# Kernel tuning notes

Measured on AMD Instinct MI355X. Metric: run time of the kernel, lower is better.

## Reference

```python
import jax, jax.numpy as jnp
import numpy as np

B = 8192       # Monte Carlo paths
NSTEP = 30     # Euler time steps
D = 100        # z_dim / number of assets
H1 = 110
H2 = 110
T = NSTEP - 1  # number of subnets
DT = np.float32(1.0 / NSTEP)
R = np.float32(0.05)   # riskfree
EPS = np.float32(1e-3) # Keras BatchNormalization epsilon


def setup_inputs() -> dict:
    key = jax.random.key(0)
    ks = jax.random.split(key, 25)
    f = jnp.float32
    X = jax.random.normal(ks[0], (B, NSTEP, D), f)
    DWs = jax.random.normal(ks[1], (B, NSTEP, D), f) * jnp.sqrt(DT)
    sigmas = jax.random.uniform(ks[2], (D,), f, 0.1, 0.4)
    y_init = jax.random.uniform(ks[3], (1,), f, 0.0, 1.0)
    z_init = jax.random.uniform(ks[4], (1, D), f, -0.1, 0.1)
    W1 = jax.random.normal(ks[5], (T, D, H1), f) / np.sqrt(D).astype(np.float32)
    W2 = jax.random.normal(ks[6], (T, H1, H2), f) / np.sqrt(H1).astype(np.float32)
    W3 = jax.random.normal(ks[7], (T, H2, D), f) / np.sqrt(H2).astype(np.float32)
    dims = [D, H1, H2, D]
    bn = {}
    for j, dim in enumerate(dims):
        bn[f"g{j}"] = 1.0 + 0.1 * jax.random.normal(ks[8 + 4 * j], (T, dim), f)
        bn[f"b{j}"] = 0.05 * jax.random.normal(ks[9 + 4 * j], (T, dim), f)
        bn[f"m{j}"] = 0.1 * jax.random.normal(ks[10 + 4 * j], (T, dim), f)
        bn[f"v{j}"] = jax.random.uniform(ks[11 + 4 * j], (T, dim), f, 0.5, 1.5)
    return dict(X=X, DWs=DWs, sigmas=sigmas, y_init=y_init, z_init=z_init,
                W1=W1, W2=W2, W3=W3, **bn)


def _bn(x, g, b, m, v):
    # Keras BatchNormalization, inference mode
    return (x - m) * jax.lax.rsqrt(v + EPS) * g + b


def _subnet(x, p):
    (w1, w2, w3, g0, b0, m0, v0, g1, b1, m1, v1,
     g2, b2, m2, v2, g3, b3, m3, v3) = p
    x = _bn(x, g0, b0, m0, v0)
    x = jax.nn.relu(x @ w1)
    x = _bn(x, g1, b1, m1, v1)
    x = jax.nn.relu(x @ w2)
    x = _bn(x, g2, b2, m2, v2)
    x = x @ w3
    return _bn(x, g3, b3, m3, v3)


def reference(X, DWs, sigmas, y_init, z_init, W1, W2, W3,
              g0, b0, m0, v0, g1, b1, m1, v1,
              g2, b2, m2, v2, g3, b3, m3, v3):
    nb = X.shape[0]
    Y0 = jnp.ones((nb, 1), X.dtype) * y_init            # [B,1]
    Z0 = jnp.ones((nb, 1), X.dtype) * z_init            # [B,D]

    def step(carry, xs):
        Y, Z = carry
        Xi, Xn, DWi, p = xs
        Y = Y + R * Y * DT + jnp.sum(sigmas * Xi * Z * DWi, axis=1, keepdims=True)
        Z = _subnet(Xn, p)
        return (Y, Z), None

    params = (W1, W2, W3, g0, b0, m0, v0, g1, b1, m1, v1,
              g2, b2, m2, v2, g3, b3, m3, v3)  # each leading dim T
    xs = (jnp.moveaxis(X[:, :T], 1, 0),        # [T,B,D]
          jnp.moveaxis(X[:, 1:T + 1], 1, 0),   # [T,B,D]
          jnp.moveaxis(DWs[:, :T], 1, 0),      # [T,B,D]
          params)
    (Y, Z), _ = jax.lax.scan(step, (Y0, Z0), xs)
    # final step: X[:,-2,:] with DWs[:,-1,:]
    Y = Y + R * Y * DT + jnp.sum(sigmas * X[:, -2, :] * Z * DWs[:, -1, :],
                                 axis=1, keepdims=True)
    return Y
```

## Files before the change

kernel.cpp:

```cpp
#include <hip/hip_runtime.h>

typedef unsigned short ushort_t;
typedef __attribute__((ext_vector_type(8))) short s16x8;
typedef __attribute__((ext_vector_type(4))) float f32x4;

#define B_PATHS 8192
#define NSTEP   30
#define DD      100
#define HH      110
#define TT      29
#define ROWSTR  3000
#define LDK     136
#define WFRAGSZ 14336
#define DT_C    (1.0f/30.0f)
#define R_C     0.05f
#define EPS_C   1e-3f

__device__ __forceinline__ ushort_t f2bf(float f) {
  unsigned u = __float_as_uint(f);
  u = u + 0x7FFFu + ((u >> 16) & 1u);
  return (ushort_t)(u >> 16);
}
__device__ __forceinline__ float bf2f(ushort_t u) {
  return __uint_as_float(((unsigned)u) << 16);
}

__global__ void prep_kernel(const float* __restrict__ W1, const float* __restrict__ W2,
                            const float* __restrict__ W3,
                            const float* g0, const float* b0, const float* m0, const float* v0,
                            const float* g1, const float* b1, const float* m1, const float* v1,
                            const float* g2, const float* b2, const float* m2, const float* v2,
                            const float* g3, const float* b3, const float* m3, const float* v3,
                            ushort_t* __restrict__ wprep, float* __restrict__ bprep)
{
  const int mat = blockIdx.x, t = blockIdx.y, tid = threadIdx.x;
  __shared__ float wsh[110*110];
  __shared__ float sin_[112], hin_[112], sout_[112], hout_[112];

  int Kr, Nr; const float* W; const float *g, *bb, *mm, *vv;
  if (mat == 0)      { Kr = 100; Nr = 110; W = W1 + t*11000; g = g0+t*100; bb = b0+t*100; mm = m0+t*100; vv = v0+t*100; }
  else if (mat == 1) { Kr = 110; Nr = 110; W = W2 + t*12100; g = g1+t*110; bb = b1+t*110; mm = m1+t*110; vv = v1+t*110; }
  else               { Kr = 110; Nr = 100; W = W3 + t*11000; g = g2+t*110; bb = b2+t*110; mm = m2+t*110; vv = v2+t*110; }

  if (tid < Kr) {
    float s = g[tid] * rsqrtf(vv[tid] + EPS_C);
    sin_[tid] = s; hin_[tid] = bb[tid] - mm[tid]*s;
  }
  if (mat == 2 && tid < Nr) {
    float s = g3[t*100+tid] * rsqrtf(v3[t*100+tid] + EPS_C);
    sout_[tid] = s; hout_[tid] = b3[t*100+tid] - m3[t*100+tid]*s;
  }
  for (int i = tid; i < Kr*Nr; i += 256) wsh[i] = W[i];
  __syncthreads();

  if (tid < 128) {
    float c = 0.f;
    if (tid < Nr) {
      for (int k = 0; k < Kr; ++k) c += hin_[k] * wsh[k*Nr + tid];
      if (mat == 2) c = c * sout_[tid] + hout_[tid];
    }
    bprep[(t*3 + mat)*128 + tid] = c;
  }

  ushort_t* wo = wprep + (size_t)(t*3 + mat) * WFRAGSZ;
  for (int ch = tid; ch < 1792; ch += 256) {
    const int lane = ch & 63, ntkb = ch >> 6;
    const int nt = ntkb % 7, kb = ntkb / 7;
    const int n  = nt*16 + (lane & 15);
    const int k0 = kb*32 + (lane >> 4)*8;
    ushort_t tmp[8];
#pragma unroll
    for (int j = 0; j < 8; ++j) {
      const int k = k0 + j;
      float v = 0.f;
      if (n < Nr && k < Kr) {
        v = sin_[k] * wsh[k*Nr + n];
        if (mat == 2) v *= sout_[n];
      }
      tmp[j] = f2bf(v);
    }
    ushort4 lo; lo.x = tmp[0]; lo.y = tmp[1]; lo.z = tmp[2]; lo.w = tmp[3];
    ushort4 hi; hi.x = tmp[4]; hi.y = tmp[5]; hi.z = tmp[6]; hi.w = tmp[7];
    *(ushort4*)(wo + ch*8)     = lo;
    *(ushort4*)(wo + ch*8 + 4) = hi;
  }
}

__device__ __forceinline__ void mlp_stage(const ushort_t* actIn, const ushort_t* __restrict__ wfrag,
                                          const float* __restrict__ biasg, ushort_t* actOut,
                                          int lane, int lrow, int quad, bool relu)
{
  f32x4 acc[7];
  const f32x4 z4 = {0.f, 0.f, 0.f, 0.f};
#pragma unroll
  for (int nt = 0; nt < 7; ++nt) acc[nt] = z4;
  s16x8 a[4];
#pragma unroll
  for (int kb = 0; kb < 4; ++kb)
    a[kb] = *(const s16x8*)(actIn + lrow*LDK + kb*32 + quad*8);
#pragma unroll
  for (int kb = 0; kb < 4; ++kb) {
#pragma unroll
    for (int nt = 0; nt < 7; ++nt) {
      s16x8 b = *(const s16x8*)(wfrag + ((kb*7 + nt)*64 + lane)*8);
      acc[nt] = __builtin_amdgcn_mfma_f32_16x16x32_bf16(a[kb], b, acc[nt], 0, 0, 0);
    }
  }
  __asm__ volatile("" ::: "memory");
#pragma unroll
  for (int nt = 0; nt < 7; ++nt) {
    const int col = nt*16 + lrow;
    const float bv = biasg[col];
#pragma unroll
    for (int r = 0; r < 4; ++r) {
      float u = acc[nt][r] + bv;
      if (relu) u = u > 0.f ? u : 0.f;
      actOut[(quad*4 + r)*LDK + col] = f2bf(u);
    }
  }
#pragma unroll
  for (int r = 0; r < 4; ++r)
    actOut[(quad*4 + r)*LDK + 112 + lrow] = 0;
  __asm__ volatile("" ::: "memory");
}

__global__ __launch_bounds__(256, 4)
void subnet_kernel(const float* __restrict__ X, const float* __restrict__ DW,
                   const float* __restrict__ sigmas,
                   const ushort_t* __restrict__ wprep, const float* __restrict__ bprep,
                   float* __restrict__ sbuf)
{
  __shared__ __align__(16) ushort_t actA[4][16*LDK];
  __shared__ __align__(16) ushort_t actB[4][16*LDK];

  const int tid  = threadIdx.x;
  const int wv   = tid >> 6;
  const int t    = blockIdx.y;
  const int m0   = blockIdx.x * 64 + wv * 16;
  const int lane = tid & 63, lrow = lane & 15, quad = lane >> 4;
  const int row16 = lane >> 2, part = lane & 3;
  const int brow  = m0 + row16;

  ushort_t* A  = actA[wv];
  ushort_t* Bq = actB[wv];

  const float* drp = DW + (size_t)brow*ROWSTR + (t+1)*DD;
  float4 dwv[7];
#pragma unroll
  for (int g = 0; g < 7; ++g) {
    const int c = part + g*4;
    if (c < 25) dwv[g] = *(const float4*)(drp + c*4);
    else        { dwv[g].x = 0.f; dwv[g].y = 0.f; dwv[g].z = 0.f; dwv[g].w = 0.f; }
  }

  const float* xrp = X + (size_t)brow*ROWSTR + (t+1)*DD;
#pragma unroll
  for (int g = 0; g < 8; ++g) {
    const int c = part + g*4;
    ushort4 u; u.x = 0; u.y = 0; u.z = 0; u.w = 0;
    if (c < 25) {
      const float4 v = *(const float4*)(xrp + c*4);
      u.x = f2bf(v.x); u.y = f2bf(v.y); u.z = f2bf(v.z); u.w = f2bf(v.w);
    }
    *(ushort4*)(A + row16*LDK + c*4) = u;
  }
  __asm__ volatile("" ::: "memory");

  const ushort_t* wf = wprep + (size_t)(t*3) * WFRAGSZ;
  const float*    bg = bprep + (t*3) * 128;

  mlp_stage(A,  wf,             bg,       Bq, lane, lrow, quad, true);
  mlp_stage(Bq, wf + WFRAGSZ,   bg + 128, A,  lane, lrow, quad, true);
  mlp_stage(A,  wf + 2*WFRAGSZ, bg + 256, Bq, lane, lrow, quad, false);

  {
    const int xt = (t == TT - 1) ? (NSTEP - 2) : (t + 1);
    const float* xe = X + (size_t)brow*ROWSTR + xt*DD;
    float p = 0.f;
#pragma unroll
    for (int g = 0; g < 7; ++g) {
      const int c = part + g*4;
      if (c < 25) {
        const float4 xv = *(const float4*)(xe + c*4);
        const float4 sg = *(const float4*)(sigmas + c*4);
        const ushort4 zu = *(const ushort4*)(Bq + row16*LDK + c*4);
        p += sg.x*xv.x*dwv[g].x*bf2f(zu.x);
        p += sg.y*xv.y*dwv[g].y*bf2f(zu.y);
        p += sg.z*xv.z*dwv[g].z*bf2f(zu.z);
        p += sg.w*xv.w*dwv[g].w*bf2f(zu.w);
      }
    }
    p += __shfl_xor(p, 1, 64);
    p += __shfl_xor(p, 2, 64);
    if (part == 0)
      sbuf[(size_t)(t+1)*B_PATHS + brow] = p;
  }
}

__global__ void y_kernel(const float* __restrict__ X, const float* __restrict__ DW,
                         const float* __restrict__ sigmas, const float* __restrict__ y_init,
                         const float* __restrict__ z_init, const float* __restrict__ sbuf,
                         float* __restrict__ out)
{
  const int b = blockIdx.x * blockDim.x + threadIdx.x;
  const float* xr = X + (size_t)b * ROWSTR;
  const float* dr = DW + (size_t)b * ROWSTR;
  float s0 = 0.f;
#pragma unroll 5
  for (int c = 0; c < 25; ++c) {
    float4 xv = *(const float4*)(xr + c*4);
    float4 dv = *(const float4*)(dr + c*4);
    float4 sg = *(const float4*)(sigmas + c*4);
    float4 zv = *(const float4*)(z_init + c*4);
    s0 += sg.x*xv.x*zv.x*dv.x;
    s0 += sg.y*xv.y*zv.y*dv.y;
    s0 += sg.z*xv.z*zv.z*dv.z;
    s0 += sg.w*xv.w*zv.w*dv.w;
  }
  float y = y_init[0];
  y = y + R_C*y*DT_C + s0;
#pragma unroll
  for (int tau = 1; tau < NSTEP; ++tau)
    y = y + R_C*y*DT_C + sbuf[(size_t)tau*B_PATHS + b];
  out[b] = y;
}

extern "C" void kernel_launch(void* const* d_in, const int* in_sizes, int n_in,
                              void* d_out, int out_size, void* d_ws, size_t ws_size,
                              hipStream_t stream) {
  const float* X      = (const float*)d_in[0];
  const float* DWs    = (const float*)d_in[1];
  const float* sigmas = (const float*)d_in[2];
  const float* y_init = (const float*)d_in[3];
  const float* z_init = (const float*)d_in[4];
  const float* W1     = (const float*)d_in[5];
  const float* W2     = (const float*)d_in[6];
  const float* W3     = (const float*)d_in[7];
  const float* bn[16];
  for (int i = 0; i < 16; ++i) bn[i] = (const float*)d_in[8 + i];

  char* ws = (char*)d_ws;
  ushort_t* wprep = (ushort_t*)ws;
  float*    bprep = (float*)(ws + 2494464);
  float*    sbuf  = (float*)(ws + 2539008);
  float*    out   = (float*)d_out;

  prep_kernel<<<dim3(3, TT), 256, 0, stream>>>(
      W1, W2, W3,
      bn[0], bn[1], bn[2], bn[3],  bn[4], bn[5], bn[6], bn[7],
      bn[8], bn[9], bn[10], bn[11], bn[12], bn[13], bn[14], bn[15],
      wprep, bprep);
  subnet_kernel<<<dim3(B_PATHS/64, TT), 256, 0, stream>>>(
      X, DWs, sigmas, wprep, bprep, sbuf);
  y_kernel<<<dim3(B_PATHS/256), 256, 0, stream>>>(
      X, DWs, sigmas, y_init, z_init, sbuf, out);
}
```

Baseline: 336.7 us.

## Process 32 rows per wave so each weight fragment feeds two MFMAs

Each wavefront now handles 32 batch rows instead of 16. Every weight fragment loaded from global memory feeds two MFMA chains, which halves weight traffic per row. Activations are updated in place in one LDS buffer per wave instead of ping-ponging between two. The DW loads move from the prologue to the epilogue, and the block count is halved with launch bounds lowered to 3 waves per EU. This raises register pressure, reduces the number of blocks, and rewrites the buffer in place, which depends on all A fragments being loaded before the stores.

```diff
diff --git a/kernel.cpp b/kernel.cpp
--- a/kernel.cpp
+++ b/kernel.cpp
@@ -86,24 +86,27 @@
   }
 }
 
-__device__ __forceinline__ void mlp_stage(const ushort_t* actIn, const ushort_t* __restrict__ wfrag,
-                                          const float* __restrict__ biasg, ushort_t* actOut,
-                                          int lane, int lrow, int quad, bool relu)
-{
-  f32x4 acc[7];
+__device__ __forceinline__ void mlp_stage32(ushort_t* act, const ushort_t* __restrict__ wfrag,
+                                            const float* __restrict__ biasg,
+                                            int lane, int lrow, int quad, bool relu)
+{
+  s16x8 aL[4], aH[4];
+#pragma unroll
+  for (int kb = 0; kb < 4; ++kb) {
+    aL[kb] = *(const s16x8*)(act + lrow*LDK + kb*32 + quad*8);
+    aH[kb] = *(const s16x8*)(act + (16 + lrow)*LDK + kb*32 + quad*8);
+  }
+  f32x4 accL[7], accH[7];
   const f32x4 z4 = {0.f, 0.f, 0.f, 0.f};
 #pragma unroll
-  for (int nt = 0; nt < 7; ++nt) acc[nt] = z4;
-  s16x8 a[4];
-#pragma unroll
-  for (int kb = 0; kb < 4; ++kb)
-    a[kb] = *(const s16x8*)(actIn + lrow*LDK + kb*32 + quad*8);
+  for (int nt = 0; nt < 7; ++nt) { accL[nt] = z4; accH[nt] = z4; }
 #pragma unroll
   for (int kb = 0; kb < 4; ++kb) {
 #pragma unroll
     for (int nt = 0; nt < 7; ++nt) {
       s16x8 b = *(const s16x8*)(wfrag + ((kb*7 + nt)*64 + lane)*8);
-      acc[nt] = __builtin_amdgcn_mfma_f32_16x16x32_bf16(a[kb], b, acc[nt], 0, 0, 0);
+      accL[nt] = __builtin_amdgcn_mfma_f32_16x16x32_bf16(aL[kb], b, accL[nt], 0, 0, 0);
+      accH[nt] = __builtin_amdgcn_mfma_f32_16x16x32_bf16(aH[kb], b, accH[nt], 0, 0, 0);
     }
   }
   __asm__ volatile("" ::: "memory");
@@ -113,86 +116,80 @@
     const float bv = biasg[col];
 #pragma unroll
     for (int r = 0; r < 4; ++r) {
-      float u = acc[nt][r] + bv;
-      if (relu) u = u > 0.f ? u : 0.f;
-      actOut[(quad*4 + r)*LDK + col] = f2bf(u);
-    }
-  }
-#pragma unroll
-  for (int r = 0; r < 4; ++r)
-    actOut[(quad*4 + r)*LDK + 112 + lrow] = 0;
+      float uL = accL[nt][r] + bv;
+      float uH = accH[nt][r] + bv;
+      if (relu) { uL = uL > 0.f ? uL : 0.f; uH = uH > 0.f ? uH : 0.f; }
+      act[(quad*4 + r)*LDK + col]        = f2bf(uL);
+      act[(16 + quad*4 + r)*LDK + col]   = f2bf(uH);
+    }
+  }
+#pragma unroll
+  for (int r = 0; r < 4; ++r) {
+    act[(quad*4 + r)*LDK + 112 + lrow]      = 0;
+    act[(16 + quad*4 + r)*LDK + 112 + lrow] = 0;
+  }
   __asm__ volatile("" ::: "memory");
 }
 
-__global__ __launch_bounds__(256, 4)
+__global__ __launch_bounds__(256, 3)
 void subnet_kernel(const float* __restrict__ X, const float* __restrict__ DW,
                    const float* __restrict__ sigmas,
                    const ushort_t* __restrict__ wprep, const float* __restrict__ bprep,
                    float* __restrict__ sbuf)
 {
-  __shared__ __align__(16) ushort_t actA[4][16*LDK];
-  __shared__ __align__(16) ushort_t actB[4][16*LDK];
+  __shared__ __align__(16) ushort_t act[4][32*LDK];
 
   const int tid  = threadIdx.x;
   const int wv   = tid >> 6;
   const int t    = blockIdx.y;
-  const int m0   = blockIdx.x * 64 + wv * 16;
+  const int m0   = blockIdx.x * 128 + wv * 32;
   const int lane = tid & 63, lrow = lane & 15, quad = lane >> 4;
-  const int row16 = lane >> 2, part = lane & 3;
-  const int brow  = m0 + row16;
-
-  ushort_t* A  = actA[wv];
-  ushort_t* Bq = actB[wv];
-
-  const float* drp = DW + (size_t)brow*ROWSTR + (t+1)*DD;
-  float4 dwv[7];
-#pragma unroll
-  for (int g = 0; g < 7; ++g) {
-    const int c = part + g*4;
-    if (c < 25) dwv[g] = *(const float4*)(drp + c*4);
-    else        { dwv[g].x = 0.f; dwv[g].y = 0.f; dwv[g].z = 0.f; dwv[g].w = 0.f; }
-  }
+  const int row2 = lane >> 1, part2 = lane & 1;
+  const int brow = m0 + row2;
+
+  ushort_t* A = act[wv];
 
   const float* xrp = X + (size_t)brow*ROWSTR + (t+1)*DD;
 #pragma unroll
-  for (int g = 0; g < 8; ++g) {
-    const int c = part + g*4;
+  for (int g = 0; g < 16; ++g) {
+    const int c = part2 + g*2;
     ushort4 u; u.x = 0; u.y = 0; u.z = 0; u.w = 0;
     if (c < 25) {
       const float4 v = *(const float4*)(xrp + c*4);
       u.x = f2bf(v.x); u.y = f2bf(v.y); u.z = f2bf(v.z); u.w = f2bf(v.w);
     }
-    *(ushort4*)(A + row16*LDK + c*4) = u;
+    *(ushort4*)(A + row2*LDK + c*4) = u;
   }
   __asm__ volatile("" ::: "memory");
 
   const ushort_t* wf = wprep + (size_t)(t*3) * WFRAGSZ;
   const float*    bg = bprep + (t*3) * 128;
 
-  mlp_stage(A,  wf,             bg,       Bq, lane, lrow, quad, true);
-  mlp_stage(Bq, wf + WFRAGSZ,   bg + 128, A,  lane, lrow, quad, true);
-  mlp_stage(A,  wf + 2*WFRAGSZ, bg + 256, Bq, lane, lrow, quad, false);
+  mlp_stage32(A, wf,             bg,       lane, lrow, quad, true);
+  mlp_stage32(A, wf + WFRAGSZ,   bg + 128, lane, lrow, quad, true);
+  mlp_stage32(A, wf + 2*WFRAGSZ, bg + 256, lane, lrow, quad, false);
 
   {
     const int xt = (t == TT - 1) ? (NSTEP - 2) : (t + 1);
-    const float* xe = X + (size_t)brow*ROWSTR + xt*DD;
+    const float* xe = X  + (size_t)brow*ROWSTR + xt*DD;
+    const float* dr = DW + (size_t)brow*ROWSTR + (t+1)*DD;
     float p = 0.f;
 #pragma unroll
-    for (int g = 0; g < 7; ++g) {
-      const int c = part + g*4;
+    for (int g = 0; g < 13; ++g) {
+      const int c = part2 + g*2;
       if (c < 25) {
         const float4 xv = *(const float4*)(xe + c*4);
+        const float4 dv = *(const float4*)(dr + c*4);
         const float4 sg = *(const float4*)(sigmas + c*4);
-        const ushort4 zu = *(const ushort4*)(Bq + row16*LDK + c*4);
-        p += sg.x*xv.x*dwv[g].x*bf2f(zu.x);
-        p += sg.y*xv.y*dwv[g].y*bf2f(zu.y);
-        p += sg.z*xv.z*dwv[g].z*bf2f(zu.z);
-        p += sg.w*xv.w*dwv[g].w*bf2f(zu.w);
+        const ushort4 zu = *(const ushort4*)(A + row2*LDK + c*4);
+        p += sg.x*xv.x*dv.x*bf2f(zu.x);
+        p += sg.y*xv.y*dv.y*bf2f(zu.y);
+        p += sg.z*xv.z*dv.z*bf2f(zu.z);
+        p += sg.w*xv.w*dv.w*bf2f(zu.w);
       }
     }
     p += __shfl_xor(p, 1, 64);
-    p += __shfl_xor(p, 2, 64);
-    if (part == 0)
+    if (part2 == 0)
       sbuf[(size_t)(t+1)*B_PATHS + brow] = p;
   }
 }
@@ -250,7 +247,7 @@
       bn[0], bn[1], bn[2], bn[3],  bn[4], bn[5], bn[6], bn[7],
       bn[8], bn[9], bn[10], bn[11], bn[12], bn[13], bn[14], bn[15],
       wprep, bprep);
-  subnet_kernel<<<dim3(B_PATHS/64, TT), 256, 0, stream>>>(
+  subnet_kernel<<<dim3(B_PATHS/128, TT), 256, 0, stream>>>(
       X, DWs, sigmas, wprep, bprep, sbuf);
   y_kernel<<<dim3(B_PATHS/256), 256, 0, stream>>>(
       X, DWs, sigmas, y_init, z_init, sbuf, out);
```

After: 349.5 us. 1.04x slower.
